# Kernel optimization log

Hardware: AMD Instinct MI355X
Metric: run time of the kernel (lower is better)

The kernel has to match this reference:

```python
import jax, jax.numpy as jnp
import numpy as np

BATCH, D, H, SLOTS = 256, 512, 2048, 32768

def setup_inputs() -> dict:
    key = jax.random.key(0)
    ks = jax.random.split(key, 8)
    s = 0.02  # weight init scale
    return {
        "S_t": jax.random.normal(ks[0], (BATCH, D), jnp.float32),
        "mem_keys": jax.random.normal(ks[1], (SLOTS, D), jnp.float32),
        "mem_vals": jax.random.normal(ks[2], (SLOTS, D), jnp.float32),
        "Wk": jax.random.normal(ks[3], (D, D), jnp.float32) * s,
        "bk": jnp.zeros((D,), jnp.float32),
        "Wv": jax.random.normal(ks[4], (D, D), jnp.float32) * s,
        "bv": jnp.zeros((D,), jnp.float32),
        "W1": jax.random.normal(ks[5], (H, 2 * D), jnp.float32) * s,
        "b1": jnp.zeros((H,), jnp.float32),
        "W2": jax.random.normal(ks[6], (D, H), jnp.float32) * s,
        "b2": jnp.zeros((D,), jnp.float32),
    }

def reference(S_t, mem_keys, mem_vals, Wk, bk, Wv, bv, W1, b1, W2, b2):
    # Sequential per-sample memory read/write (write at step i affects read at i+1)
    def step(carry, s_i):
        mk, mv = carry                       # [SLOTS, D] each
        k = s_i @ Wk.T + bk                  # key projection [D]
        scores = mk @ k                      # [SLOTS] similarity (gather-side)
        attn = jax.nn.softmax(scores)
        read_val = attn @ mv                 # content-addressed read [D]
        # write: scatter key/value into best-matching slot
        wv = s_i @ Wv.T + bv
        slot = jnp.argmax(scores)
        mk = mk.at[slot].set(k)
        mv = mv.at[slot].set(wv)
        merged = jnp.concatenate([s_i, read_val])   # [2D]
        delta = jax.nn.relu(merged @ W1.T + b1) @ W2.T + b2
        return (mk, mv), delta

    (_, _), deltas = jax.lax.scan(step, (mem_keys, mem_vals), S_t)
    return deltas  # [BATCH, D]
```

## Files before the change

### kernel.cpp

```cpp
#include <hip/hip_runtime.h>
#include <cstdint>
#include <cstddef>

#define BATCH 256
#define DIM   512
#define HIDN  2048
#define SLOTS 32768
#define NCHUNK 4
#define CHSZ  (SLOTS/NCHUNK)

typedef __attribute__((ext_vector_type(8))) short short8;
typedef __attribute__((ext_vector_type(8))) _Float16 half8;
typedef __attribute__((ext_vector_type(4))) float f32x4;

__device__ __forceinline__ unsigned short bf_rne(float x) {
  unsigned int u = __float_as_uint(x);
  unsigned int r = (u + 0x7fffu + ((u >> 16) & 1u)) >> 16;
  return (unsigned short)r;
}
__device__ __forceinline__ unsigned short bf_split(float x, float& rem) {
  unsigned short h = bf_rne(x);
  rem = x - __uint_as_float(((unsigned int)h) << 16);
  return h;
}
__device__ __forceinline__ unsigned int pack2(unsigned short a, unsigned short b) {
  return (unsigned int)a | ((unsigned int)b << 16);
}

__device__ __forceinline__ unsigned short h_rne(float x) {
  _Float16 h = (_Float16)x;
  union { _Float16 f; unsigned short u; } cv; cv.f = h;
  return cv.u;
}
__device__ __forceinline__ unsigned short h_split(float x, float& rem) {
  _Float16 h = (_Float16)x;
  rem = x - (float)h;
  union { _Float16 f; unsigned short u; } cv; cv.f = h;
  return cv.u;
}

__device__ __forceinline__ void gemm64_body(
    const float* __restrict__ A, int lda, const float* __restrict__ B, int ldb,
    const float* __restrict__ bias, float* __restrict__ C, int ldc,
    int K, int relu, int addC,
    unsigned short* __restrict__ hi, unsigned short* __restrict__ lo,
    int bx, int by, int t, float (*As)[68], float (*Bs)[68])
{
  const int m0 = bx * 64;
  const int n0 = by * 64;
  const int tx = t & 15, ty = t >> 4;
  const int lr = t >> 2;
  const int lc = (t & 3) * 4;
  float acc[4][4] = {};
  for (int k0 = 0; k0 < K; k0 += 16) {
    float4 a = *(const float4*)(A + (size_t)(m0 + lr) * lda + k0 + lc);
    float4 b = *(const float4*)(B + (size_t)(n0 + lr) * ldb + k0 + lc);
    __syncthreads();
    As[lc+0][lr] = a.x; As[lc+1][lr] = a.y; As[lc+2][lr] = a.z; As[lc+3][lr] = a.w;
    Bs[lc+0][lr] = b.x; Bs[lc+1][lr] = b.y; Bs[lc+2][lr] = b.z; Bs[lc+3][lr] = b.w;
    __syncthreads();
    #pragma unroll
    for (int k = 0; k < 16; ++k) {
      const float4 a4 = *(const float4*)&As[k][ty*4];
      const float4 b4 = *(const float4*)&Bs[k][tx*4];
      const float aa[4] = {a4.x, a4.y, a4.z, a4.w};
      const float bb[4] = {b4.x, b4.y, b4.z, b4.w};
      #pragma unroll
      for (int u = 0; u < 4; ++u)
        #pragma unroll
        for (int v = 0; v < 4; ++v)
          acc[u][v] = fmaf(aa[u], bb[v], acc[u][v]);
    }
  }
  #pragma unroll
  for (int u = 0; u < 4; ++u) {
    const int m = m0 + ty*4 + u;
    float o[4];
    #pragma unroll
    for (int v = 0; v < 4; ++v) {
      float c = acc[u][v];
      if (addC) c += C[(size_t)m * ldc + n0 + tx*4 + v];
      if (bias) c += bias[n0 + tx*4 + v];
      if (relu) c = fmaxf(c, 0.0f);
      o[v] = c;
    }
    *(float4*)(C + (size_t)m * ldc + n0 + tx*4) = make_float4(o[0], o[1], o[2], o[3]);
    if (hi) {
      float r0, r1, r2, r3;
      unsigned short h0 = bf_split(o[0], r0), h1 = bf_split(o[1], r1);
      unsigned short h2 = bf_split(o[2], r2), h3 = bf_split(o[3], r3);
      *(uint2*)(hi + (size_t)m * ldc + n0 + tx*4) =
          make_uint2(pack2(h0, h1), pack2(h2, h3));
      *(uint2*)(lo + (size_t)m * ldc + n0 + tx*4) =
          make_uint2(pack2(bf_rne(r0), bf_rne(r1)), pack2(bf_rne(r2), bf_rne(r3)));
    }
  }
}

__global__ __launch_bounds__(256) void gemm_bt(
    const float* __restrict__ A, int lda, const float* __restrict__ B, int ldb,
    const float* __restrict__ bias, float* __restrict__ C, int ldc,
    int K, int relu, int addC)
{
  __shared__ __align__(16) float As[16][68];
  __shared__ __align__(16) float Bs[16][68];
  gemm64_body(A, lda, B, ldb, bias, C, ldc, K, relu, addC, nullptr, nullptr,
              blockIdx.x, blockIdx.y, threadIdx.x, As, Bs);
}

__global__ __launch_bounds__(256) void proj2(
    const float* __restrict__ S_t,
    const float* __restrict__ Wk, const float* __restrict__ bk, float* __restrict__ Kp,
    unsigned short* __restrict__ Khi, unsigned short* __restrict__ Klo,
    const float* __restrict__ Wv, const float* __restrict__ bv, float* __restrict__ WVp)
{
  __shared__ __align__(16) float As[16][68];
  __shared__ __align__(16) float Bs[16][68];
  int b = blockIdx.x;
  if (b < 32)
    gemm64_body(S_t, 512, Wk, 512, bk, Kp, 512, 512, 0, 0, Khi, Klo,
                b & 3, b >> 2, threadIdx.x, As, Bs);
  else {
    b -= 32;
    gemm64_body(S_t, 512, Wv, 512, bv, WVp, 512, 512, 0, 0, nullptr, nullptr,
                b & 3, b >> 2, threadIdx.x, As, Bs);
  }
}

#define LSTR 40
__device__ __forceinline__ void mfma_scores_body(
    const unsigned short* __restrict__ Ahi, const unsigned short* __restrict__ Alo,
    const float* __restrict__ B, float* __restrict__ C, int M, int N, int K,
    int bx, int by, int t,
    unsigned short* sAhi, unsigned short* sAlo,
    unsigned short* sBhi, unsigned short* sBlo)
{
  const int m0 = bx * 128, n0 = by * 128;
  const int wave = t >> 6, lane = t & 63;
  const int wr = (wave >> 1) * 64, wc = (wave & 1) * 64;
  const int lrow = lane & 15, quad = lane >> 4;
  const int sr = t >> 1;
  const int sc = (t & 1) * 16;

  f32x4 acc[4][4];
  #pragma unroll
  for (int a = 0; a < 4; ++a)
    #pragma unroll
    for (int b = 0; b < 4; ++b)
      acc[a][b] = (f32x4){0.f, 0.f, 0.f, 0.f};

  for (int k0 = 0; k0 < K; k0 += 32) {
    const size_t aoff = (size_t)(m0 + sr) * K + k0 + sc;
    uint4 ah0 = *(const uint4*)(Ahi + aoff);
    uint4 ah1 = *(const uint4*)(Ahi + aoff + 8);
    uint4 al0 = *(const uint4*)(Alo + aoff);
    uint4 al1 = *(const uint4*)(Alo + aoff + 8);
    const float* bp = B + (size_t)(n0 + sr) * K + k0 + sc;
    float4 b0 = *(const float4*)(bp + 0);
    float4 b1 = *(const float4*)(bp + 4);
    float4 b2 = *(const float4*)(bp + 8);
    float4 b3 = *(const float4*)(bp + 12);
    float bx_[16] = {b0.x,b0.y,b0.z,b0.w, b1.x,b1.y,b1.z,b1.w,
                     b2.x,b2.y,b2.z,b2.w, b3.x,b3.y,b3.z,b3.w};
    unsigned short bh[16], bl[16];
    #pragma unroll
    for (int e = 0; e < 16; ++e) {
      float rem; bh[e] = bf_split(bx_[e], rem); bl[e] = bf_rne(rem);
    }
    __syncthreads();
    *(uint4*)&sAhi[sr*LSTR + sc]     = ah0;
    *(uint4*)&sAhi[sr*LSTR + sc + 8] = ah1;
    *(uint4*)&sAlo[sr*LSTR + sc]     = al0;
    *(uint4*)&sAlo[sr*LSTR + sc + 8] = al1;
    *(uint4*)&sBhi[sr*LSTR + sc] =
        make_uint4(pack2(bh[0],bh[1]), pack2(bh[2],bh[3]),
                   pack2(bh[4],bh[5]), pack2(bh[6],bh[7]));
    *(uint4*)&sBhi[sr*LSTR + sc + 8] =
        make_uint4(pack2(bh[8],bh[9]), pack2(bh[10],bh[11]),
                   pack2(bh[12],bh[13]), pack2(bh[14],bh[15]));
    *(uint4*)&sBlo[sr*LSTR + sc] =
        make_uint4(pack2(bl[0],bl[1]), pack2(bl[2],bl[3]),
                   pack2(bl[4],bl[5]), pack2(bl[6],bl[7]));
    *(uint4*)&sBlo[sr*LSTR + sc + 8] =
        make_uint4(pack2(bl[8],bl[9]), pack2(bl[10],bl[11]),
                   pack2(bl[12],bl[13]), pack2(bl[14],bl[15]));
    __syncthreads();

    short8 afh[4], afl[4], bfh[4], bfl[4];
    #pragma unroll
    for (int mt = 0; mt < 4; ++mt) {
      const int ar = wr + mt*16 + lrow;
      afh[mt] = *(const short8*)&sAhi[ar*LSTR + quad*8];
      afl[mt] = *(const short8*)&sAlo[ar*LSTR + quad*8];
    }
    #pragma unroll
    for (int nt = 0; nt < 4; ++nt) {
      const int br = wc + nt*16 + lrow;
      bfh[nt] = *(const short8*)&sBhi[br*LSTR + quad*8];
      bfl[nt] = *(const short8*)&sBlo[br*LSTR + quad*8];
    }
    #pragma unroll
    for (int mt = 0; mt < 4; ++mt)
      #pragma unroll
      for (int nt = 0; nt < 4; ++nt) {
        acc[mt][nt] = __builtin_amdgcn_mfma_f32_16x16x32_bf16(afh[mt], bfh[nt], acc[mt][nt], 0, 0, 0);
        acc[mt][nt] = __builtin_amdgcn_mfma_f32_16x16x32_bf16(afl[mt], bfh[nt], acc[mt][nt], 0, 0, 0);
        acc[mt][nt] = __builtin_amdgcn_mfma_f32_16x16x32_bf16(afh[mt], bfl[nt], acc[mt][nt], 0, 0, 0);
      }
  }
  #pragma unroll
  for (int mt = 0; mt < 4; ++mt)
    #pragma unroll
    for (int nt = 0; nt < 4; ++nt)
      #pragma unroll
      for (int reg = 0; reg < 4; ++reg) {
        const int m = m0 + wr + mt*16 + quad*4 + reg;
        const int n = n0 + wc + nt*16 + lrow;
        C[(size_t)m * N + n] = acc[mt][nt][reg];
      }
}

__global__ __launch_bounds__(256) void gram_scores(
    const float* __restrict__ Kp, float* __restrict__ G,
    const unsigned short* __restrict__ Khi, const unsigned short* __restrict__ Klo,
    const float* __restrict__ mem_keys, float* __restrict__ S0T)
{
  __shared__ __align__(16) unsigned char arena[40960];
  const int b = blockIdx.x;
  if (b < 16) {
    float (*As)[68] = (float (*)[68])arena;
    float (*Bs)[68] = (float (*)[68])(arena + 4352);
    gemm64_body(Kp, 512, Kp, 512, nullptr, G, 256, 512, 0, 0, nullptr, nullptr,
                b & 3, b >> 2, threadIdx.x, As, Bs);
  } else {
    const int sb = b - 16;
    unsigned short* sAhi = (unsigned short*)arena;
    unsigned short* sAlo = (unsigned short*)(arena + 10240);
    unsigned short* sBhi = (unsigned short*)(arena + 20480);
    unsigned short* sBlo = (unsigned short*)(arena + 30720);
    mfma_scores_body(Khi, Klo, mem_keys, S0T, 256, 32768, 512,
                     sb & 1, sb >> 1, threadIdx.x, sAhi, sAlo, sBhi, sBlo);
  }
}

__global__ __launch_bounds__(256) void colchunk_gtop(
    const float* __restrict__ S0T, float* __restrict__ cmax,
    float* __restrict__ cse, float* __restrict__ c16v, int* __restrict__ c16i,
    const float* __restrict__ G, float* __restrict__ gv16, int* __restrict__ gj16)
{
  __shared__ float redv[4]; __shared__ int redi[4];
  __shared__ float outv[16]; __shared__ int outi[16];
  __shared__ float ws2[4];
  __shared__ float gvals[BATCH];
  const int t = threadIdx.x;

  if (blockIdx.x >= 1024) {
    const int i = blockIdx.x - 1024;
    const int lane = t & 63, w = t >> 6;
    gvals[t] = (t < i) ? G[(size_t)i*BATCH + t] : -1e30f;
    __syncthreads();
    for (int r = 0; r < 16; ++r) {
      float bv = gvals[t]; int bj = t;
      #pragma unroll
      for (int off = 32; off; off >>= 1) {
        float ov = __shfl_xor(bv, off); int oj = __shfl_xor(bj, off);
        if (ov > bv || (ov == bv && oj < bj)) { bv = ov; bj = oj; }
      }
      if (lane == 0) { redv[w] = bv; redi[w] = bj; }
      __syncthreads();
      if (t == 0) {
        float fv = redv[0]; int fj = redi[0];
        #pragma unroll
        for (int w2 = 1; w2 < 4; ++w2)
          if (redv[w2] > fv || (redv[w2] == fv && redi[w2] < fj)) { fv = redv[w2]; fj = redi[w2]; }
        gv16[i*16 + r] = fv; gj16[i*16 + r] = fj;
        gvals[fj] = -1e30f;
      }
      __syncthreads();
    }
    return;
  }

  const int ch = blockIdx.x & 3, row = blockIdx.x >> 2;
  const float* col = S0T + (size_t)row * SLOTS + ch * CHSZ;
  const int base = t * (CHSZ / 256);
  float v[16]; int ix[16];
  #pragma unroll
  for (int q = 0; q < 16; ++q) { v[q] = -1e30f; ix[q] = 0x7fffffff; }
  #pragma unroll
  for (int u = 0; u < 32; u += 4) {
    float4 x4 = *(const float4*)(col + base + u);
    float xs[4] = {x4.x, x4.y, x4.z, x4.w};
    #pragma unroll
    for (int e = 0; e < 4; ++e) {
      float cv = xs[e]; int ci = ch * CHSZ + base + u + e;
      if (cv > v[15] || (cv == v[15] && ci < ix[15])) {
        #pragma unroll
        for (int q = 0; q < 16; ++q) {
          bool better = (cv > v[q]) || (cv == v[q] && ci < ix[q]);
          float tv = better ? v[q] : cv;
          int   ti = better ? ix[q] : ci;
          v[q]  = better ? cv : v[q];
          ix[q] = better ? ci : ix[q];
          cv = tv; ci = ti;
        }
      }
    }
  }
  for (int r = 0; r < 16; ++r) {
    float bv = v[0]; int bi = ix[0];
    #pragma unroll
    for (int off = 32; off; off >>= 1) {
      float ov = __shfl_xor(bv, off); int oi = __shfl_xor(bi, off);
      if (ov > bv || (ov == bv && oi < bi)) { bv = ov; bi = oi; }
    }
    if ((t & 63) == 0) { redv[t >> 6] = bv; redi[t >> 6] = bi; }
    __syncthreads();
    float fv = redv[0]; int fi = redi[0];
    #pragma unroll
    for (int w = 1; w < 4; ++w)
      if (redv[w] > fv || (redv[w] == fv && redi[w] < fi)) { fv = redv[w]; fi = redi[w]; }
    if (t == 0) { outv[r] = fv; outi[r] = fi; }
    const bool adv = (v[0] == fv) && (ix[0] == fi);
    #pragma unroll
    for (int q = 0; q < 15; ++q) {
      v[q]  = adv ? v[q+1]  : v[q];
      ix[q] = adv ? ix[q+1] : ix[q];
    }
    v[15]  = adv ? -1e30f     : v[15];
    ix[15] = adv ? 0x7fffffff : ix[15];
    __syncthreads();
  }
  const int cidx = row * NCHUNK + ch;
  if (t < 16) { c16v[cidx*16 + t] = outv[t]; c16i[cidx*16 + t] = outi[t]; }
  const float m = outv[0];
  float s = 0.f;
  #pragma unroll
  for (int u = 0; u < 32; u += 4) {
    float4 x4 = *(const float4*)(col + base + u);
    s += __expf(x4.x - m) + __expf(x4.y - m) + __expf(x4.z - m) + __expf(x4.w - m);
  }
  #pragma unroll
  for (int off = 32; off; off >>= 1) s += __shfl_xor(s, off);
  if ((t & 63) == 0) ws2[t >> 6] = s;
  __syncthreads();
  if (t == 0) { cse[cidx] = ws2[0]+ws2[1]+ws2[2]+ws2[3]; cmax[cidx] = m; }
}

__global__ __launch_bounds__(64) void col_combine(
    const float* __restrict__ cmax, const float* __restrict__ cse,
    const float* __restrict__ c16v, const int* __restrict__ c16i,
    float* __restrict__ m_base, float* __restrict__ se_base,
    float* __restrict__ t16v, int* __restrict__ t16i)
{
  const int i = blockIdx.x, lane = threadIdx.x;
  float v = c16v[(size_t)i * 64 + lane];
  int   id = c16i[(size_t)i * 64 + lane];
  float m0 = cmax[i*4+0], m1 = cmax[i*4+1], m2 = cmax[i*4+2], m3 = cmax[i*4+3];
  const float m = fmaxf(fmaxf(m0, m1), fmaxf(m2, m3));
  const float se = cse[i*4+0]*__expf(m0-m) + cse[i*4+1]*__expf(m1-m)
                 + cse[i*4+2]*__expf(m2-m) + cse[i*4+3]*__expf(m3-m);
  bool dead = false;
  for (int r = 0; r < 16; ++r) {
    float bv = dead ? -1e30f : v;
    int   bi = dead ? 0x7fffffff : id;
    #pragma unroll
    for (int off = 32; off; off >>= 1) {
      float ov = __shfl_xor(bv, off); int oi = __shfl_xor(bi, off);
      if (ov > bv || (ov == bv && oi < bi)) { bv = ov; bi = oi; }
    }
    if (!dead && v == bv && id == bi) dead = true;
    if (lane == 0) { t16v[i*16 + r] = bv; t16i[i*16 + r] = bi; }
  }
  if (lane == 0) { m_base[i] = m; se_base[i] = se; }
}

#define EXP_SCALE 16384.0f
#define KCHUNK 1024
__global__ __launch_bounds__(256) void seq_plus_gemm(
    const float* __restrict__ S0T, const float* __restrict__ G,
    const float* __restrict__ t16v, const int* __restrict__ t16i,
    const float* __restrict__ gv16, const int* __restrict__ gj16,
    int* __restrict__ slots,
    const float* __restrict__ B, const float* __restrict__ mArr,
    float* __restrict__ part,
    const float* __restrict__ S_t, const float* __restrict__ W1,
    float* __restrict__ hid)
{
  __shared__ __align__(16) unsigned char smem[70656];

  if (blockIdx.x == 0) {
    unsigned int* bitmap = (unsigned int*)smem;
    float* sv       = (float*)(smem + 4096);
    int*   si       = (int*)  (smem + 20480);
    float* gv       = (float*)(smem + 36864);
    int*   gj       = (int*)  (smem + 53248);
    int*   slots_sh = (int*)  (smem + 69632);
    volatile unsigned int* vbm = bitmap;
    const int tt = threadIdx.x;
    for (int q = tt; q < SLOTS/32; q += 256) bitmap[q] = 0u;
    for (int q = tt; q < BATCH*16; q += 256) {
      sv[q] = t16v[q]; si[q] = t16i[q]; gv[q] = gv16[q]; gj[q] = gj16[q];
    }
    __syncthreads();
    if (tt < 64) {
      const int lane = tt;
      unsigned long long alive[4] = {0ull,0ull,0ull,0ull};
      int slotr0 = -1, slotr1 = -1, slotr2 = -1, slotr3 = -1;

      float myv = -1e30f; int myslot = 0; unsigned int wpref = 0;
      float ovq = -1e30f; int ojq = 0;
      if (lane < 16) {
        myv = sv[lane]; myslot = si[lane];
        wpref = vbm[myslot >> 5];
        ovq = gv[lane]; ojq = gj[lane];
      }
      int prev_slot = -1;

      for (int i = 0; i < BATCH; ++i) {
        bool bvalid = false, ovalid = false;
        if (lane < 16) {
          bvalid = (((wpref >> (myslot & 31)) & 1u) == 0u) && (myslot != prev_slot);
          unsigned long long am = (ojq < 64) ? alive[0] : (ojq < 128) ? alive[1]
                                 : (ojq < 192) ? alive[2] : alive[3];
          ovalid = (ovq > -1e29f) && (((am >> (ojq & 63)) & 1ull) != 0ull);
        }
        unsigned long long bb = __ballot(bvalid);
        unsigned long long ob = __ballot(ovalid);

        float myv_n = -1e30f; int myslot_n = 0; unsigned int wpref_n = 0;
        float ovq_n = -1e30f; int ojq_n = 0;
        if (i + 1 < BATCH && lane < 16) {
          myv_n = sv[(i+1)*16 + lane]; myslot_n = si[(i+1)*16 + lane];
          wpref_n = vbm[myslot_n >> 5];
          ovq_n = gv[(i+1)*16 + lane]; ojq_n = gj[(i+1)*16 + lane];
        }

        float bval; int bslot;
        if (bb != 0ull) {
          int bl = __ffsll((unsigned long long)bb) - 1;
          bval = __shfl(myv, bl); bslot = __shfl(myslot, bl);
        } else {
          float fv = -1e30f; int fi = 0x7fffffff;
          for (int s = lane; s < SLOTS; s += 64) {
            if (((vbm[s >> 5] >> (s & 31)) & 1u) == 0u) {
              float x = S0T[(size_t)i*SLOTS + s];
              if (x > fv || (x == fv && s < fi)) { fv = x; fi = s; }
            }
          }
          #pragma unroll
          for (int off = 32; off; off >>= 1) {
            float ovv = __shfl_xor(fv, off); int oii = __shfl_xor(fi, off);
            if (ovv > fv || (ovv == fv && oii < fi)) { fv = ovv; fi = oii; }
          }
          bval = fv; bslot = fi;
        }

        float oval = -1e30f; int oslot = 0x7fffffff;
        if (ob != 0ull) {
          int ol = __ffsll((unsigned long long)ob) - 1;
          oval = __shfl(ovq, ol);
          int ojw = __shfl(ojq, ol);
          int r = ojw >> 6;
          int srg = (r == 0) ? slotr0 : (r == 1) ? slotr1 : (r == 2) ? slotr2 : slotr3;
          oslot = __shfl(srg, ojw & 63);
        } else if ((alive[0] | alive[1] | alive[2] | alive[3]) != 0ull) {
          float fv = -1e30f; int fj = 0x7fffffff;
          #pragma unroll
          for (int r = 0; r < 4; ++r) {
            int j = lane + 64*r;
            if (j < i && ((alive[r] >> lane) & 1ull)) {
              float x = G[(size_t)i*BATCH + j];
              if (x > fv || (x == fv && j < fj)) { fv = x; fj = j; }
            }
          }
          #pragma unroll
          for (int off = 32; off; off >>= 1) {
            float ovv = __shfl_xor(fv, off); int ojj = __shfl_xor(fj, off);
            if (ovv > fv || (ovv == fv && ojj < fj)) { fv = ovv; fj = ojj; }
          }
          if (fj != 0x7fffffff) {
            oval = fv;
            int r = fj >> 6;
            int srg = (r == 0) ? slotr0 : (r == 1) ? slotr1 : (r == 2) ? slotr2 : slotr3;
            oslot = __shfl(srg, fj & 63);
          }
        }

        const bool owins = (oval > bval) || (oval == bval && oslot < bslot);
        const int sloti = owins ? oslot : bslot;

        unsigned long long kb0 = __ballot(slotr0 == sloti);
        unsigned long long kb1 = __ballot(slotr1 == sloti);
        unsigned long long kb2 = __ballot(slotr2 == sloti);
        unsigned long long kb3 = __ballot(slotr3 == sloti);
        alive[0] &= ~kb0; alive[1] &= ~kb1; alive[2] &= ~kb2; alive[3] &= ~kb3;
        const int r_new = i >> 6;
        if (lane == (i & 63)) {
          if (r_new == 0) slotr0 = sloti;
          else if (r_new == 1) slotr1 = sloti;
          else if (r_new == 2) slotr2 = sloti;
          else slotr3 = sloti;
        }
        alive[r_new] |= (1ull << (i & 63));
        if (lane == 0) {
          slots_sh[i] = sloti;
          vbm[sloti >> 5] = vbm[sloti >> 5] | (1u << (sloti & 31));
        }
        prev_slot = sloti;
        myv = myv_n; myslot = myslot_n; wpref = wpref_n; ovq = ovq_n; ojq = ojq_n;
        __builtin_amdgcn_wave_barrier();
      }
      for (int q = lane; q < BATCH; q += 64) slots[q] = slots_sh[q];
    }
    return;
  }

  if (blockIdx.x >= 257) {
    float (*As)[68] = (float (*)[68])smem;
    float (*Bs)[68] = (float (*)[68])(smem + 4352);
    const int b2 = blockIdx.x - 257;
    gemm64_body(S_t, 512, W1, 1024, nullptr, hid, 2048, 512, 0, 0, nullptr, nullptr,
                b2 & 3, b2 >> 2, threadIdx.x, As, Bs);
    return;
  }

  unsigned short* sAhi = (unsigned short*)smem;
  unsigned short* sAlo = (unsigned short*)(smem + 10240);
  unsigned short* sBhi = (unsigned short*)(smem + 20480);
  unsigned short* sBlo = (unsigned short*)(smem + 29184);

  const int b  = blockIdx.x - 1;
  const int bx = b >> 7;
  const int by = (b >> 5) & 3;
  const int bz = b & 31;
  const int m0 = bx * 128, n0 = by * 128;
  const int kb = bz * KCHUNK;
  const int t = threadIdx.x;
  const int wave = t >> 6, lane = t & 63;
  const int wr = (wave >> 1) * 64, wc = (wave & 1) * 64;
  const int lrow = lane & 15, quad = lane >> 4;
  const int sr = t >> 1;
  const int sc = (t & 1) * 16;
  const int pr = t >> 4;
  const int nbase = (t & 15) * 8;
  const float mrow = mArr[m0 + sr];

  f32x4 acc[4][4];
  #pragma unroll
  for (int a = 0; a < 4; ++a)
    #pragma unroll
    for (int c = 0; c < 4; ++c)
      acc[a][c] = (f32x4){0.f, 0.f, 0.f, 0.f};

  for (int k0 = kb; k0 < kb + KCHUNK; k0 += 32) {
    const float* ap = S0T + (size_t)(m0 + sr) * SLOTS + k0 + sc;
    float4 a0 = *(const float4*)(ap);
    float4 a1 = *(const float4*)(ap + 4);
    float4 a2 = *(const float4*)(ap + 8);
    float4 a3 = *(const float4*)(ap + 12);
    const float* bp = B + (size_t)(k0 + 2*pr) * DIM + n0 + nbase;
    float4 q0 = *(const float4*)(bp);
    float4 q1 = *(const float4*)(bp + 4);
    float4 q2 = *(const float4*)(bp + DIM);
    float4 q3 = *(const float4*)(bp + DIM + 4);

    float ax[16] = {a0.x,a0.y,a0.z,a0.w, a1.x,a1.y,a1.z,a1.w,
                    a2.x,a2.y,a2.z,a2.w, a3.x,a3.y,a3.z,a3.w};
    unsigned short ah[16], av[16];
    #pragma unroll
    for (int e = 0; e < 16; ++e) {
      float rm; float ee = __expf(ax[e] - mrow) * EXP_SCALE;
      ah[e] = h_split(ee, rm); av[e] = h_rne(rm);
    }
    float r0[8] = {q0.x,q0.y,q0.z,q0.w, q1.x,q1.y,q1.z,q1.w};
    float r1[8] = {q2.x,q2.y,q2.z,q2.w, q3.x,q3.y,q3.z,q3.w};
    unsigned int pbh[8], pbl[8];
    #pragma unroll
    for (int e = 0; e < 8; ++e) {
      float rm0, rm1;
      unsigned short h0 = h_split(r0[e], rm0);
      unsigned short h1 = h_split(r1[e], rm1);
      pbh[e] = pack2(h0, h1);
      pbl[e] = pack2(h_rne(rm0), h_rne(rm1));
    }

    __syncthreads();
    *(uint4*)&sAhi[sr*LSTR + sc] =
        make_uint4(pack2(ah[0],ah[1]), pack2(ah[2],ah[3]),
                   pack2(ah[4],ah[5]), pack2(ah[6],ah[7]));
    *(uint4*)&sAhi[sr*LSTR + sc + 8] =
        make_uint4(pack2(ah[8],ah[9]), pack2(ah[10],ah[11]),
                   pack2(ah[12],ah[13]), pack2(ah[14],ah[15]));
    *(uint4*)&sAlo[sr*LSTR + sc] =
        make_uint4(pack2(av[0],av[1]), pack2(av[2],av[3]),
                   pack2(av[4],av[5]), pack2(av[6],av[7]));
    *(uint4*)&sAlo[sr*LSTR + sc + 8] =
        make_uint4(pack2(av[8],av[9]), pack2(av[10],av[11]),
                   pack2(av[12],av[13]), pack2(av[14],av[15]));
    {
      unsigned int* bh32 = (unsigned int*)sBhi;
      unsigned int* bl32 = (unsigned int*)sBlo;
      #pragma unroll
      for (int e = 0; e < 8; ++e) bh32[(nbase + e)*17 + pr] = pbh[e];
      #pragma unroll
      for (int e = 0; e < 8; ++e) bl32[(nbase + e)*17 + pr] = pbl[e];
    }
    __syncthreads();

    half8 afh[4], afl[4], bfh[4], bfl[4];
    #pragma unroll
    for (int mt = 0; mt < 4; ++mt) {
      const int ar = wr + mt*16 + lrow;
      afh[mt] = *(const half8*)&sAhi[ar*LSTR + quad*8];
      afl[mt] = *(const half8*)&sAlo[ar*LSTR + quad*8];
    }
    #pragma unroll
    for (int nt = 0; nt < 4; ++nt) {
      const int br = wc + nt*16 + lrow;
      const unsigned int* ph = (const unsigned int*)sBhi + br*17 + quad*4;
      const unsigned int* pl = (const unsigned int*)sBlo + br*17 + quad*4;
      union FU { unsigned int u[4]; half8 s; };
      FU th, tl;
      th.u[0] = ph[0]; th.u[1] = ph[1]; th.u[2] = ph[2]; th.u[3] = ph[3];
      tl.u[0] = pl[0]; tl.u[1] = pl[1]; tl.u[2] = pl[2]; tl.u[3] = pl[3];
      bfh[nt] = th.s; bfl[nt] = tl.s;
    }
    #pragma unroll
    for (int mt = 0; mt < 4; ++mt)
      #pragma unroll
      for (int nt = 0; nt < 4; ++nt) {
        acc[mt][nt] = __builtin_amdgcn_mfma_f32_16x16x32_f16(afh[mt], bfh[nt], acc[mt][nt], 0, 0, 0);
        acc[mt][nt] = __builtin_amdgcn_mfma_f32_16x16x32_f16(afl[mt], bfh[nt], acc[mt][nt], 0, 0, 0);
        acc[mt][nt] = __builtin_amdgcn_mfma_f32_16x16x32_f16(afh[mt], bfl[nt], acc[mt][nt], 0, 0, 0);
      }
  }
  float* Cz = part + (size_t)bz * BATCH * DIM;
  #pragma unroll
  for (int mt = 0; mt < 4; ++mt)
    #pragma unroll
    for (int nt = 0; nt < 4; ++nt)
      #pragma unroll
      for (int reg = 0; reg < 4; ++reg) {
        const int m = m0 + wr + mt*16 + quad*4 + reg;
        const int n = n0 + wc + nt*16 + lrow;
        Cz[(size_t)m * DIM + n] = acc[mt][nt][reg];
      }
}

__global__ __launch_bounds__(256) void coef_readval(
    const float* __restrict__ S0T, const float* __restrict__ G,
    const int* __restrict__ slots,
    const float* __restrict__ m_base, const float* __restrict__ se_base,
    const float* __restrict__ WVp, const float* __restrict__ mem_vals,
    const float* __restrict__ S_t, const float* __restrict__ part,
    float* __restrict__ merged)
{
  const int i = blockIdx.x, j = threadIdx.x;
  __shared__ int sh[BATCH];
  __shared__ float sca[BATCH], scs[BATCH];
  __shared__ float red[4];
  __shared__ float sh_invZ, sh_rs;
  sh[j] = slots[j];
  __syncthreads();
  const int sj = sh[j];
  int nj = 0x7fffffff;
  for (int k = j + 1; k < BATCH; ++k)
    if (sh[k] == sj) { nj = k; break; }

  const bool alive = (j < i) && (nj >= i);
  const float g = alive ? G[(size_t)i*BATCH + j] : -1e30f;
  float bv = g;
  #pragma unroll
  for (int off = 32; off; off >>= 1) bv = fmaxf(bv, __shfl_xor(bv, off));
  if ((j & 63) == 0) red[j >> 6] = bv;
  __syncthreads();
  const float mb = m_base[i];
  const float mi = fmaxf(fmaxf(fmaxf(red[0], red[1]), fmaxf(red[2], red[3])), mb);
  const float sv_ = alive ? S0T[(size_t)i*SLOTS + sj] : 0.f;
  const float ca = alive ? __expf(g - mi) : 0.f;
  const float cs = alive ? __expf(sv_ - mi) : 0.f;
  sca[j] = ca; scs[j] = cs;
  float z = ca - cs;
  #pragma unroll
  for (int off = 32; off; off >>= 1) z += __shfl_xor(z, off);
  __syncthreads();
  if ((j & 63) == 0) red[j >> 6] = z;
  __syncthreads();
  if (j == 0) {
    const float Z = se_base[i] * __expf(mb - mi) + red[0] + red[1] + red[2] + red[3];
    sh_invZ = 1.0f / Z;
    sh_rs = __expf(mb - mi) * (1.0f / EXP_SCALE);
  }
  __syncthreads();

  merged[(size_t)i*1024 + j]        = S_t[(size_t)i*DIM + j];
  merged[(size_t)i*1024 + 256 + j]  = S_t[(size_t)i*DIM + 256 + j];
  float acc0 = 0.f, acc1 = 0.f;
  #pragma unroll 4
  for (int zz = 0; zz < 32; ++zz) {
    acc0 += part[(size_t)zz * (BATCH*DIM) + (size_t)i*DIM + j];
    acc1 += part[(size_t)zz * (BATCH*DIM) + (size_t)i*DIM + 256 + j];
  }
  acc0 *= sh_rs; acc1 *= sh_rs;
  for (int jj = 0; jj < BATCH; ++jj) {
    float caj = sca[jj];
    float csj = scs[jj];
    if (caj != 0.f || csj != 0.f) {
      int sjj = sh[jj];
      acc0 += caj * WVp[(size_t)jj*DIM + j]       - csj * mem_vals[(size_t)sjj*DIM + j];
      acc1 += caj * WVp[(size_t)jj*DIM + 256 + j] - csj * mem_vals[(size_t)sjj*DIM + 256 + j];
    }
  }
  merged[(size_t)i*1024 + 512 + j] = acc0 * sh_invZ;
  merged[(size_t)i*1024 + 768 + j] = acc1 * sh_invZ;
}

extern "C" void kernel_launch(void* const* d_in, const int* in_sizes, int n_in,
                              void* d_out, int out_size, void* d_ws, size_t ws_size,
                              hipStream_t stream)
{
  (void)in_sizes; (void)n_in; (void)out_size; (void)ws_size;
  const float* S_t      = (const float*)d_in[0];
  const float* mem_keys = (const float*)d_in[1];
  const float* mem_vals = (const float*)d_in[2];
  const float* Wk       = (const float*)d_in[3];
  const float* bk       = (const float*)d_in[4];
  const float* Wv       = (const float*)d_in[5];
  const float* bv       = (const float*)d_in[6];
  const float* W1       = (const float*)d_in[7];
  const float* b1       = (const float*)d_in[8];
  const float* W2       = (const float*)d_in[9];
  const float* b2       = (const float*)d_in[10];
  float* out = (float*)d_out;

  float* ws = (float*)d_ws;
  float* Kp       = ws + 0;
  float* WVp      = ws + 131072;
  float* G        = ws + 262144;
  float* S0T      = ws + 327680;
  float* m_base   = ws + 8716288;
  float* se_base  = ws + 8716544;
  float* t16v     = ws + 8716800;
  int*   t16i     = (int*)(ws + 8720896);
  float* gv16     = ws + 8724992;
  int*   gj16     = (int*)(ws + 8729088);
  int*   slots    = (int*)(ws + 8733184);
  float* merged   = ws + 8996352;
  float* hid      = ws + 9258496;
  float* part     = ws + 9782784;
  float* cmaxb    = ws + 9782784;
  float* cseb     = ws + 9783808;
  float* c16vb    = ws + 9784832;
  int*   c16ib    = (int*)(ws + 9801216);
  unsigned short* Khi = (unsigned short*)(ws + 13977088);
  unsigned short* Klo = (unsigned short*)(ws + 14042624);

  proj2<<<dim3(64), dim3(256), 0, stream>>>(S_t, Wk, bk, Kp, Khi, Klo, Wv, bv, WVp);
  gram_scores<<<dim3(528), dim3(256), 0, stream>>>(Kp, G, Khi, Klo, mem_keys, S0T);

  colchunk_gtop<<<dim3(1280), dim3(256), 0, stream>>>(S0T, cmaxb, cseb, c16vb, c16ib,
                                                      G, gv16, gj16);
  col_combine<<<dim3(256), dim3(64), 0, stream>>>(cmaxb, cseb, c16vb, c16ib,
                                                  m_base, se_base, t16v, t16i);

  seq_plus_gemm<<<dim3(385), dim3(256), 0, stream>>>(S0T, G, t16v, t16i, gv16, gj16,
                                                     slots, mem_vals, m_base, part,
                                                     S_t, W1, hid);

  coef_readval<<<dim3(256), dim3(256), 0, stream>>>(S0T, G, slots, m_base, se_base,
                                                    WVp, mem_vals, S_t, part, merged);

  gemm_bt<<<dim3(4, 32), dim3(256), 0, stream>>>(merged + 512, 1024, W1 + 512, 1024,
                                                 b1, hid, 2048, 512, 1, 1);
  gemm_bt<<<dim3(4, 8),  dim3(256), 0, stream>>>(hid, 2048, W2, 2048,
                                                 b2, out, 512, 2048, 0, 0);
}
```

Before: 756.0 us.

## Split-K final GEMM with atomics, prefetch G rows, reuse column loads, trim readval loop

The final W2 GEMM, which had only 32 blocks, becomes a split-K launch of 128 blocks that accumulate into an output pre-filled with the bias by extra blocks added to coef_readval. The sequential kernel now prefetches the next G row into registers so the wave does not wait on a global load each step. colchunk_gtop keeps its column values in registers for the softmax-sum pass instead of reading them again. The coef_readval accumulation loop stops at i and drops its zero-coefficient branch. Float atomics make the output summation order nondeterministic.

```diff
diff --git a/kernel.cpp b/kernel.cpp
--- a/kernel.cpp
+++ b/kernel.cpp
@@ -42,7 +42,7 @@
 __device__ __forceinline__ void gemm64_body(
     const float* __restrict__ A, int lda, const float* __restrict__ B, int ldb,
     const float* __restrict__ bias, float* __restrict__ C, int ldc,
-    int K, int relu, int addC,
+    int kb, int ke, int relu, int addC, int atomic,
     unsigned short* __restrict__ hi, unsigned short* __restrict__ lo,
     int bx, int by, int t, float (*As)[68], float (*Bs)[68])
 {
@@ -52,7 +52,7 @@
   const int lr = t >> 2;
   const int lc = (t & 3) * 4;
   float acc[4][4] = {};
-  for (int k0 = 0; k0 < K; k0 += 16) {
+  for (int k0 = kb; k0 < ke; k0 += 16) {
     float4 a = *(const float4*)(A + (size_t)(m0 + lr) * lda + k0 + lc);
     float4 b = *(const float4*)(B + (size_t)(n0 + lr) * ldb + k0 + lc);
     __syncthreads();
@@ -75,24 +75,30 @@
   #pragma unroll
   for (int u = 0; u < 4; ++u) {
     const int m = m0 + ty*4 + u;
-    float o[4];
-    #pragma unroll
-    for (int v = 0; v < 4; ++v) {
-      float c = acc[u][v];
-      if (addC) c += C[(size_t)m * ldc + n0 + tx*4 + v];
-      if (bias) c += bias[n0 + tx*4 + v];
-      if (relu) c = fmaxf(c, 0.0f);
-      o[v] = c;
-    }
-    *(float4*)(C + (size_t)m * ldc + n0 + tx*4) = make_float4(o[0], o[1], o[2], o[3]);
-    if (hi) {
-      float r0, r1, r2, r3;
-      unsigned short h0 = bf_split(o[0], r0), h1 = bf_split(o[1], r1);
-      unsigned short h2 = bf_split(o[2], r2), h3 = bf_split(o[3], r3);
-      *(uint2*)(hi + (size_t)m * ldc + n0 + tx*4) =
-          make_uint2(pack2(h0, h1), pack2(h2, h3));
-      *(uint2*)(lo + (size_t)m * ldc + n0 + tx*4) =
-          make_uint2(pack2(bf_rne(r0), bf_rne(r1)), pack2(bf_rne(r2), bf_rne(r3)));
+    if (atomic) {
+      #pragma unroll
+      for (int v = 0; v < 4; ++v)
+        atomicAdd(&C[(size_t)m * ldc + n0 + tx*4 + v], acc[u][v]);
+    } else {
+      float o[4];
+      #pragma unroll
+      for (int v = 0; v < 4; ++v) {
+        float c = acc[u][v];
+        if (addC) c += C[(size_t)m * ldc + n0 + tx*4 + v];
+        if (bias) c += bias[n0 + tx*4 + v];
+        if (relu) c = fmaxf(c, 0.0f);
+        o[v] = c;
+      }
+      *(float4*)(C + (size_t)m * ldc + n0 + tx*4) = make_float4(o[0], o[1], o[2], o[3]);
+      if (hi) {
+        float r0, r1, r2, r3;
+        unsigned short h0 = bf_split(o[0], r0), h1 = bf_split(o[1], r1);
+        unsigned short h2 = bf_split(o[2], r2), h3 = bf_split(o[3], r3);
+        *(uint2*)(hi + (size_t)m * ldc + n0 + tx*4) =
+            make_uint2(pack2(h0, h1), pack2(h2, h3));
+        *(uint2*)(lo + (size_t)m * ldc + n0 + tx*4) =
+            make_uint2(pack2(bf_rne(r0), bf_rne(r1)), pack2(bf_rne(r2), bf_rne(r3)));
+      }
     }
   }
 }
@@ -104,8 +110,19 @@
 {
   __shared__ __align__(16) float As[16][68];
   __shared__ __align__(16) float Bs[16][68];
-  gemm64_body(A, lda, B, ldb, bias, C, ldc, K, relu, addC, nullptr, nullptr,
+  gemm64_body(A, lda, B, ldb, bias, C, ldc, 0, K, relu, addC, 0, nullptr, nullptr,
               blockIdx.x, blockIdx.y, threadIdx.x, As, Bs);
+}
+
+__global__ __launch_bounds__(256) void gemm_bt_sk(
+    const float* __restrict__ A, int lda, const float* __restrict__ B, int ldb,
+    float* __restrict__ C, int ldc, int kchunk)
+{
+  __shared__ __align__(16) float As[16][68];
+  __shared__ __align__(16) float Bs[16][68];
+  const int kb = blockIdx.z * kchunk;
+  gemm64_body(A, lda, B, ldb, nullptr, C, ldc, kb, kb + kchunk, 0, 0, 1,
+              nullptr, nullptr, blockIdx.x, blockIdx.y, threadIdx.x, As, Bs);
 }
 
 __global__ __launch_bounds__(256) void proj2(
@@ -118,11 +135,11 @@
   __shared__ __align__(16) float Bs[16][68];
   int b = blockIdx.x;
   if (b < 32)
-    gemm64_body(S_t, 512, Wk, 512, bk, Kp, 512, 512, 0, 0, Khi, Klo,
+    gemm64_body(S_t, 512, Wk, 512, bk, Kp, 512, 0, 512, 0, 0, 0, Khi, Klo,
                 b & 3, b >> 2, threadIdx.x, As, Bs);
   else {
     b -= 32;
-    gemm64_body(S_t, 512, Wv, 512, bv, WVp, 512, 512, 0, 0, nullptr, nullptr,
+    gemm64_body(S_t, 512, Wv, 512, bv, WVp, 512, 0, 512, 0, 0, 0, nullptr, nullptr,
                 b & 3, b >> 2, threadIdx.x, As, Bs);
   }
 }
@@ -230,7 +247,7 @@
   if (b < 16) {
     float (*As)[68] = (float (*)[68])arena;
     float (*Bs)[68] = (float (*)[68])(arena + 4352);
-    gemm64_body(Kp, 512, Kp, 512, nullptr, G, 256, 512, 0, 0, nullptr, nullptr,
+    gemm64_body(Kp, 512, Kp, 512, nullptr, G, 256, 0, 512, 0, 0, 0, nullptr, nullptr,
                 b & 3, b >> 2, threadIdx.x, As, Bs);
   } else {
     const int sb = b - 16;
@@ -284,16 +301,18 @@
   const int ch = blockIdx.x & 3, row = blockIdx.x >> 2;
   const float* col = S0T + (size_t)row * SLOTS + ch * CHSZ;
   const int base = t * (CHSZ / 256);
+  float4 xa[8];
+  #pragma unroll
+  for (int u = 0; u < 8; ++u) xa[u] = *(const float4*)(col + base + u*4);
   float v[16]; int ix[16];
   #pragma unroll
   for (int q = 0; q < 16; ++q) { v[q] = -1e30f; ix[q] = 0x7fffffff; }
   #pragma unroll
-  for (int u = 0; u < 32; u += 4) {
-    float4 x4 = *(const float4*)(col + base + u);
-    float xs[4] = {x4.x, x4.y, x4.z, x4.w};
+  for (int u = 0; u < 8; ++u) {
+    float xs[4] = {xa[u].x, xa[u].y, xa[u].z, xa[u].w};
     #pragma unroll
     for (int e = 0; e < 4; ++e) {
-      float cv = xs[e]; int ci = ch * CHSZ + base + u + e;
+      float cv = xs[e]; int ci = ch * CHSZ + base + u*4 + e;
       if (cv > v[15] || (cv == v[15] && ci < ix[15])) {
         #pragma unroll
         for (int q = 0; q < 16; ++q) {
@@ -336,9 +355,9 @@
   const float m = outv[0];
   float s = 0.f;
   #pragma unroll
-  for (int u = 0; u < 32; u += 4) {
-    float4 x4 = *(const float4*)(col + base + u);
-    s += __expf(x4.x - m) + __expf(x4.y - m) + __expf(x4.z - m) + __expf(x4.w - m);
+  for (int u = 0; u < 8; ++u) {
+    s += __expf(xa[u].x - m) + __expf(xa[u].y - m)
+       + __expf(xa[u].z - m) + __expf(xa[u].w - m);
   }
   #pragma unroll
   for (int off = 32; off; off >>= 1) s += __shfl_xor(s, off);
@@ -416,6 +435,9 @@
         ovq = gv[lane]; ojq = gj[lane];
       }
       int prev_slot = -1;
+      float grow[4];
+      #pragma unroll
+      for (int r = 0; r < 4; ++r) grow[r] = G[(size_t)0 * BATCH + lane + 64*r];
 
       for (int i = 0; i < BATCH; ++i) {
         bool bvalid = false, ovalid = false;
@@ -434,6 +456,12 @@
           myv_n = sv[(i+1)*16 + lane]; myslot_n = si[(i+1)*16 + lane];
           wpref_n = vbm[myslot_n >> 5];
           ovq_n = gv[(i+1)*16 + lane]; ojq_n = gj[(i+1)*16 + lane];
+        }
+        float grow_n[4];
+        {
+          const int nrow = (i + 1 < BATCH) ? (i + 1) : i;
+          #pragma unroll
+          for (int r = 0; r < 4; ++r) grow_n[r] = G[(size_t)nrow * BATCH + lane + 64*r];
         }
 
         float bval; int bslot;
@@ -470,7 +498,7 @@
           for (int r = 0; r < 4; ++r) {
             int j = lane + 64*r;
             if (j < i && ((alive[r] >> lane) & 1ull)) {
-              float x = G[(size_t)i*BATCH + j];
+              float x = grow[r];
               if (x > fv || (x == fv && j < fj)) { fv = x; fj = j; }
             }
           }
@@ -509,6 +537,8 @@
         }
         prev_slot = sloti;
         myv = myv_n; myslot = myslot_n; wpref = wpref_n; ovq = ovq_n; ojq = ojq_n;
+        #pragma unroll
+        for (int r = 0; r < 4; ++r) grow[r] = grow_n[r];
         __builtin_amdgcn_wave_barrier();
       }
       for (int q = lane; q < BATCH; q += 64) slots[q] = slots_sh[q];
@@ -520,8 +550,8 @@
     float (*As)[68] = (float (*)[68])smem;
     float (*Bs)[68] = (float (*)[68])(smem + 4352);
     const int b2 = blockIdx.x - 257;
-    gemm64_body(S_t, 512, W1, 1024, nullptr, hid, 2048, 512, 0, 0, nullptr, nullptr,
-                b2 & 3, b2 >> 2, threadIdx.x, As, Bs);
+    gemm64_body(S_t, 512, W1, 1024, nullptr, hid, 2048, 0, 512, 0, 0, 0,
+                nullptr, nullptr, b2 & 3, b2 >> 2, threadIdx.x, As, Bs);
     return;
   }
 
@@ -654,9 +684,21 @@
     const float* __restrict__ m_base, const float* __restrict__ se_base,
     const float* __restrict__ WVp, const float* __restrict__ mem_vals,
     const float* __restrict__ S_t, const float* __restrict__ part,
-    float* __restrict__ merged)
-{
-  const int i = blockIdx.x, j = threadIdx.x;
+    float* __restrict__ merged,
+    const float* __restrict__ bias2, float* __restrict__ outp)
+{
+  const int j = threadIdx.x;
+  if (blockIdx.x >= BATCH) {
+    const int b2 = blockIdx.x - BATCH;
+    const float z0 = bias2[j], z1 = bias2[256 + j];
+    for (int r = 0; r < 32; ++r) {
+      const int m = b2 * 32 + r;
+      outp[(size_t)m * DIM + j] = z0;
+      outp[(size_t)m * DIM + 256 + j] = z1;
+    }
+    return;
+  }
+  const int i = blockIdx.x;
   __shared__ int sh[BATCH];
   __shared__ float sca[BATCH], scs[BATCH];
   __shared__ float red[4];
@@ -703,14 +745,13 @@
     acc1 += part[(size_t)zz * (BATCH*DIM) + (size_t)i*DIM + 256 + j];
   }
   acc0 *= sh_rs; acc1 *= sh_rs;
-  for (int jj = 0; jj < BATCH; ++jj) {
-    float caj = sca[jj];
-    float csj = scs[jj];
-    if (caj != 0.f || csj != 0.f) {
-      int sjj = sh[jj];
-      acc0 += caj * WVp[(size_t)jj*DIM + j]       - csj * mem_vals[(size_t)sjj*DIM + j];
-      acc1 += caj * WVp[(size_t)jj*DIM + 256 + j] - csj * mem_vals[(size_t)sjj*DIM + 256 + j];
-    }
+  #pragma unroll 4
+  for (int jj = 0; jj < i; ++jj) {
+    const float caj = sca[jj];
+    const float csj = scs[jj];
+    const int sjj = sh[jj];
+    acc0 += caj * WVp[(size_t)jj*DIM + j]       - csj * mem_vals[(size_t)sjj*DIM + j];
+    acc1 += caj * WVp[(size_t)jj*DIM + 256 + j] - csj * mem_vals[(size_t)sjj*DIM + 256 + j];
   }
   merged[(size_t)i*1024 + 512 + j] = acc0 * sh_invZ;
   merged[(size_t)i*1024 + 768 + j] = acc1 * sh_invZ;
@@ -768,11 +809,12 @@
                                                      slots, mem_vals, m_base, part,
                                                      S_t, W1, hid);
 
-  coef_readval<<<dim3(256), dim3(256), 0, stream>>>(S0T, G, slots, m_base, se_base,
-                                                    WVp, mem_vals, S_t, part, merged);
+  coef_readval<<<dim3(264), dim3(256), 0, stream>>>(S0T, G, slots, m_base, se_base,
+                                                    WVp, mem_vals, S_t, part, merged,
+                                                    b2, out);
 
   gemm_bt<<<dim3(4, 32), dim3(256), 0, stream>>>(merged + 512, 1024, W1 + 512, 1024,
                                                  b1, hid, 2048, 512, 1, 1);
-  gemm_bt<<<dim3(4, 8),  dim3(256), 0, stream>>>(hid, 2048, W2, 2048,
-                                                 b2, out, 512, 2048, 0, 0);
-}
+  gemm_bt_sk<<<dim3(4, 8, 4), dim3(256), 0, stream>>>(hid, 2048, W2, 2048,
+                                                      out, 512, 512);
+}
```

Result: faster. 644.4 us (-14.8%).
